# Kernel optimization log

Measured on AMD Instinct MI355X. Metric: run time of the kernel, lower is better.

## Reference

```python
import jax, jax.numpy as jnp
import numpy as np

B, N, K, E = 2, 131072, 20, 256  # batch, points, n_slot, feat/embed dim
GN_GROUPS = 4
IOU_THR = 0.5
SCORE_THR = 0.04
TEMP = 0.05


def setup_inputs() -> dict:
    key = jax.random.key(0)
    ks = jax.random.split(key, 6)
    wscale = 1.0 / np.sqrt(E)
    return {
        "features": jax.random.normal(ks[0], (B, N, E), jnp.float32),
        "slots": jax.random.normal(ks[1], (B, K, E), jnp.float32),
        "w1": jax.random.normal(ks[2], (E, E), jnp.float32) * wscale,
        "b1": jax.random.normal(ks[3], (E,), jnp.float32) * 0.01,
        "gn_g": jnp.ones((E,), jnp.float32),
        "gn_b": jnp.zeros((E,), jnp.float32),
        "w2": jax.random.normal(ks[4], (E, E), jnp.float32) * wscale,
        "b2": jax.random.normal(ks[5], (E,), jnp.float32) * 0.01,
    }


def _l2norm(x, axis):
    n = jnp.linalg.norm(x, axis=axis, keepdims=True)
    return x / jnp.maximum(n, 1e-12)  # F.normalize semantics


def _nms_filter(mask):
    # mask: [N, K] soft instance probabilities (rows sum to 1)
    scores = mask.mean(axis=0)                       # [K]
    valid = scores >= SCORE_THR
    order = jnp.argsort(-scores)                     # descending score
    sm = mask[:, order]                              # [N, K] sorted columns
    bm = (sm > 0.5).astype(mask.dtype).T             # [K, N] binary masks
    areas = bm.sum(axis=1)                           # [K]
    inter = bm @ bm.T                                # [K, K] pairwise intersections
    union = areas[:, None] + areas[None, :] - inter
    iou = inter / (union + 1e-8)
    idx = jnp.arange(K)
    sup0 = ~valid[order]                             # invalid slots pre-suppressed

    def body(i, sup):
        keep_i = ~sup[i]
        return sup | (keep_i & (iou[i] > IOU_THR) & (idx > i))

    sup = jax.lax.fori_loop(0, K, body, sup0)
    kept = ~sup                                      # [K]
    # kept columns are packed (in score order) into the left of the output;
    # dropped columns are routed to a dump column K which is sliced away.
    pos = jnp.cumsum(kept) - 1
    cols = jnp.where(kept, pos, K)
    out = jnp.zeros((mask.shape[0], K + 1), mask.dtype).at[:, cols].set(sm)
    out = out[:, :K]
    # per-point renormalization over kept masks (zeros stay zero if none kept)
    return out / (out.sum(axis=1, keepdims=True) + 1e-8)


def reference(features, slots, w1, b1, gn_g, gn_b, w2, b2):
    # object_mlp: Conv1d(1x1) -> GroupNorm(4) -> ReLU -> Conv1d(1x1)
    x = jnp.einsum('bke,oe->bok', slots, w1) + b1[None, :, None]   # [B, E, K]
    xg = x.reshape(B, GN_GROUPS, E // GN_GROUPS, K)
    mu = xg.mean(axis=(2, 3), keepdims=True)
    var = xg.var(axis=(2, 3), keepdims=True)
    xg = (xg - mu) * jax.lax.rsqrt(var + 1e-5)
    x = xg.reshape(B, E, K) * gn_g[None, :, None] + gn_b[None, :, None]
    x = jax.nn.relu(x)
    slot = jnp.einsum('bek,fe->bfk', x, w2) + b2[None, :, None]    # [B, F=E, K]

    fn = _l2norm(features, axis=-1)                                # [B, N, E]
    sn = _l2norm(slot, axis=1)                                     # [B, E, K]
    logits = jnp.einsum('bnd,bdk->bnk', fn, sn) / TEMP
    mask = jax.nn.softmax(logits, axis=-1)                         # [B, N, K]

    out = jax.vmap(_nms_filter)(mask)                              # [B, N, K]
    return out.transpose(0, 2, 1)                                  # [B, K, N]
```

## Files before the change

### kernel.cpp

```cpp
#include <hip/hip_runtime.h>

#define B_ 2
#define N_ 131072
#define K_ 20
#define E_ 256
#define TEMP_ 0.05f
#define SCORE_THR_ 0.04f

#define WS_SCORE 0
#define WS_XN    1024
#define WS_SN    16384
#define WS_MASK  32768
#define WS_SPART 6291456

typedef __attribute__((ext_vector_type(8))) short short8;
typedef __attribute__((ext_vector_type(4))) float f32x4;

__device__ inline float wave_sum(float v) {
    #pragma unroll
    for (int off = 32; off; off >>= 1) v += __shfl_xor(v, off, 64);
    return v;
}

__device__ inline void cvt_hilo(const float4 a, const float4 b, short8& h, short8& l) {
    float f[8] = {a.x, a.y, a.z, a.w, b.x, b.y, b.z, b.w};
    #pragma unroll
    for (int j = 0; j < 8; ++j) {
        const unsigned u  = __float_as_uint(f[j]);
        const unsigned hb = (u + 0x7fffu + ((u >> 16) & 1u)) & 0xffff0000u;
        h[j] = (short)(hb >> 16);
        const float r = f[j] - __uint_as_float(hb);
        const unsigned v = __float_as_uint(r);
        l[j] = (short)((v + 0x7fffu + ((v >> 16) & 1u)) >> 16);
    }
}

__global__ __launch_bounds__(256) void kA1(const float* __restrict__ slots,
                                           const float* __restrict__ w1,
                                           const float* __restrict__ b1,
                                           const float* __restrict__ gn_g,
                                           const float* __restrict__ gn_b,
                                           float* __restrict__ ws) {
    __shared__ __align__(16) float slds[20 * 260];
    __shared__ float red[2];
    const int t = threadIdx.x;
    const int b = blockIdx.x >> 2, g = blockIdx.x & 3;
    if (t < 2) red[t] = 0.f;
    const float* sb = slots + (size_t)b * K_ * E_;
    #pragma unroll
    for (int i = 0; i < 20; ++i) slds[i * 260 + t] = sb[i * 256 + t];
    __syncthreads();

    const int c = t >> 2, q = t & 3;
    const int o = g * 64 + c;
    const float* w1r = w1 + (size_t)o * E_;
    float acc[5] = {0.f, 0.f, 0.f, 0.f, 0.f};
    for (int e4 = 0; e4 < 64; ++e4) {
        const float4 w4 = *(const float4*)(w1r + e4 * 4);
        #pragma unroll
        for (int kk = 0; kk < 5; ++kk) {
            const float4 s4 = *(const float4*)&slds[(q * 5 + kk) * 260 + e4 * 4];
            acc[kk] += w4.x * s4.x + w4.y * s4.y + w4.z * s4.z + w4.w * s4.w;
        }
    }
    const float bias = b1[o];
    float s1 = 0.f, s2 = 0.f;
    #pragma unroll
    for (int kk = 0; kk < 5; ++kk) {
        acc[kk] += bias;
        s1 += acc[kk];
        s2 += acc[kk] * acc[kk];
    }
    s1 = wave_sum(s1);
    s2 = wave_sum(s2);
    if ((t & 63) == 0) { atomicAdd(&red[0], s1); atomicAdd(&red[1], s2); }
    __syncthreads();
    const float mean = red[0] * (1.f / 1280.f);
    const float var  = red[1] * (1.f / 1280.f) - mean * mean;
    const float rstd = rsqrtf(var + 1e-5f);
    const float gg = gn_g[o], gb = gn_b[o];
    float* xn = ws + WS_XN + (size_t)b * K_ * E_;
    #pragma unroll
    for (int kk = 0; kk < 5; ++kk) {
        float v = (acc[kk] - mean) * rstd * gg + gb;
        v = v > 0.f ? v : 0.f;
        xn[(q * 5 + kk) * 256 + o] = v;
    }
}

__global__ __launch_bounds__(256) void kA2(const float* __restrict__ w2,
                                           const float* __restrict__ b2,
                                           float* __restrict__ ws) {
    __shared__ __align__(16) float xv[256];
    __shared__ float wred[4];
    const int t = threadIdx.x;
    const int b = blockIdx.x / 20, k = blockIdx.x % 20;
    const float* xn = ws + WS_XN + (size_t)(b * 20 + k) * 256;
    xv[t] = xn[t];
    __syncthreads();
    const float* w2r = w2 + (size_t)t * 256;
    float acc = 0.f;
    for (int e4 = 0; e4 < 64; ++e4) {
        const float4 w4 = *(const float4*)(w2r + e4 * 4);
        const float4 x4 = *(const float4*)&xv[e4 * 4];
        acc += w4.x * x4.x + w4.y * x4.y + w4.z * x4.z + w4.w * x4.w;
    }
    acc += b2[t];
    float sq = wave_sum(acc * acc);
    if ((t & 63) == 0) wred[t >> 6] = sq;
    __syncthreads();
    const float nsq = wred[0] + wred[1] + wred[2] + wred[3];
    const float inv = 1.f / fmaxf(sqrtf(nsq), 1e-12f);
    ws[WS_SN + (size_t)(b * 20 + k) * 256 + t] = acc * inv;
}

__global__ __launch_bounds__(256, 2) void kB(const float* __restrict__ feat,
                                             float* __restrict__ ws) {
    __shared__ short8 sfh[2][8][64];
    __shared__ short8 sfl[2][8][64];
    __shared__ float wsum[4][20];
    const int t = threadIdx.x;
    const int lane = t & 63, w = t >> 6;
    const int b = blockIdx.x >> 9, blk = blockIdx.x & 511;
    const int s = lane & 15, g = lane >> 4;

    {
        #pragma unroll
        for (int i = 0; i < 4; ++i) {
            const int combo = w * 4 + i;
            const int tile = combo >> 3, ks = combo & 7;
            const int slot = tile * 16 + s;
            short8 h, l;
            if (slot < K_) {
                const float* snp = ws + WS_SN + ((size_t)(b * K_ + slot)) * E_
                                 + ks * 32 + g * 8;
                cvt_hilo(*(const float4*)snp, *(const float4*)(snp + 4), h, l);
            } else {
                #pragma unroll
                for (int j = 0; j < 8; ++j) { h[j] = 0; l[j] = 0; }
            }
            sfh[tile][ks][lane] = h;
            sfl[tile][ks][lane] = l;
        }
    }
    __syncthreads();

    const float* fp0 = feat + ((size_t)b * N_ + blk * 256 + s) * E_;
    float sreg0 = 0.f, sreg1 = 0.f;

    for (int it = 0; it < 4; ++it) {
        const int pb = w * 64 + it * 16;
        const float* fp = fp0 + (size_t)pb * E_;
        f32x4 c0 = {0.f, 0.f, 0.f, 0.f};
        f32x4 c1 = {0.f, 0.f, 0.f, 0.f};
        float nr = 0.f;
        #pragma unroll
        for (int ks = 0; ks < 8; ++ks) {
            const float* q = fp + ks * 32 + g * 8;
            const float4 a  = *(const float4*)q;
            const float4 bb = *(const float4*)(q + 4);
            nr += a.x * a.x + a.y * a.y + a.z * a.z + a.w * a.w
                + bb.x * bb.x + bb.y * bb.y + bb.z * bb.z + bb.w * bb.w;
            short8 fh, fl;
            cvt_hilo(a, bb, fh, fl);
            const short8 sh0 = sfh[0][ks][lane], sl0 = sfl[0][ks][lane];
            const short8 sh1 = sfh[1][ks][lane], sl1 = sfl[1][ks][lane];
            c0 = __builtin_amdgcn_mfma_f32_16x16x32_bf16(fh, sh0, c0, 0, 0, 0);
            c1 = __builtin_amdgcn_mfma_f32_16x16x32_bf16(fh, sh1, c1, 0, 0, 0);
            c0 = __builtin_amdgcn_mfma_f32_16x16x32_bf16(fh, sl0, c0, 0, 0, 0);
            c1 = __builtin_amdgcn_mfma_f32_16x16x32_bf16(fh, sl1, c1, 0, 0, 0);
            c0 = __builtin_amdgcn_mfma_f32_16x16x32_bf16(fl, sh0, c0, 0, 0, 0);
            c1 = __builtin_amdgcn_mfma_f32_16x16x32_bf16(fl, sh1, c1, 0, 0, 0);
        }
        nr += __shfl_xor(nr, 16, 64);
        nr += __shfl_xor(nr, 32, 64);
        const float scl = rsqrtf(fmaxf(nr, 1e-24f)) * (1.f / TEMP_);

        float p0[4], p1[4];
        #pragma unroll
        for (int r = 0; r < 4; ++r) {
            const float sr = __shfl(scl, 4 * g + r, 64);
            const float x0 = c0[r] * sr;
            const float x1 = c1[r] * sr;
            float m = (s < 4) ? fmaxf(x0, x1) : x0;
            #pragma unroll
            for (int off = 1; off < 16; off <<= 1) m = fmaxf(m, __shfl_xor(m, off, 64));
            const float e0 = __expf(x0 - m);
            const float e1 = (s < 4) ? __expf(x1 - m) : 0.f;
            float su = e0 + e1;
            #pragma unroll
            for (int off = 1; off < 16; off <<= 1) su += __shfl_xor(su, off, 64);
            const float inv = 1.f / su;
            p0[r] = e0 * inv;
            p1[r] = e1 * inv;
        }
        const int col = blk * 256 + pb + 4 * g;
        float* mrow = ws + WS_MASK + ((size_t)b * K_ + s) * N_ + col;
        *(float4*)mrow = make_float4(p0[0], p0[1], p0[2], p0[3]);
        sreg0 += p0[0] + p0[1] + p0[2] + p0[3];
        if (s < 4) {
            float* mrow1 = ws + WS_MASK + ((size_t)b * K_ + 16 + s) * N_ + col;
            *(float4*)mrow1 = make_float4(p1[0], p1[1], p1[2], p1[3]);
            sreg1 += p1[0] + p1[1] + p1[2] + p1[3];
        }
    }

    sreg0 += __shfl_xor(sreg0, 16, 64);
    sreg0 += __shfl_xor(sreg0, 32, 64);
    sreg1 += __shfl_xor(sreg1, 16, 64);
    sreg1 += __shfl_xor(sreg1, 32, 64);
    if (lane < 16) wsum[w][lane] = sreg0;
    if (lane < 4)  wsum[w][16 + lane] = sreg1;
    __syncthreads();
    if (t < 20)
        ws[WS_SPART + (size_t)blockIdx.x * 20 + t] =
            wsum[0][t] + wsum[1][t] + wsum[2][t] + wsum[3][t];
}

__global__ __launch_bounds__(64) void kC(float* __restrict__ ws) {
    const int l = threadIdx.x;
    const int b = blockIdx.x / 20, k = blockIdx.x % 20;
    const float* sp = ws + WS_SPART;
    float sum = 0.f;
    #pragma unroll
    for (int i = 0; i < 8; ++i)
        sum += sp[(size_t)(b * 512 + l + i * 64) * 20 + k];
    sum = wave_sum(sum);
    if (l == 0) ws[WS_SCORE + blockIdx.x] = sum * (1.f / (float)N_);
}

__global__ __launch_bounds__(256) void kD(const float* __restrict__ ws,
                                          float* __restrict__ out) {
    __shared__ float sc[20];
    __shared__ int rnk[20];
    __shared__ int src[20];
    __shared__ int nk_s;
    const int t = threadIdx.x;
    const int b = blockIdx.x >> 9;
    const int n = (blockIdx.x & 511) * 256 + t;
    if (t < 20) sc[t] = ws[WS_SCORE + b * 20 + t];
    if (t == 0) nk_s = 0;
    __syncthreads();
    if (t < 20) {
        const float mys = sc[t];
        int rank = 0;
        for (int j = 0; j < 20; ++j) {
            const float o = sc[j];
            rank += (o > mys) || (o == mys && j < t);
        }
        rnk[t] = rank;
    }
    __syncthreads();
    if (t < 20 && sc[t] >= SCORE_THR_) {
        int pos = 0;
        for (int j = 0; j < 20; ++j)
            pos += (sc[j] >= SCORE_THR_) && (rnk[j] < rnk[t]);
        src[pos] = t;
        atomicAdd(&nk_s, 1);
    }
    __syncthreads();
    const int nk = nk_s;
    const float* mg = ws + WS_MASK + (size_t)b * 20 * N_;
    float mv[20];
    float den = 1e-8f;
    #pragma unroll
    for (int p = 0; p < 20; ++p) {
        float v = 0.f;
        if (p < nk) v = mg[(size_t)src[p] * N_ + n];
        mv[p] = v;
        den += v;
    }
    const float r = 1.f / den;
    float* og = out + (size_t)b * 20 * N_ + n;
    #pragma unroll
    for (int p = 0; p < 20; ++p) og[(size_t)p * N_] = (p < nk) ? mv[p] * r : 0.f;
}

extern "C" void kernel_launch(void* const* d_in, const int* in_sizes, int n_in,
                              void* d_out, int out_size, void* d_ws, size_t ws_size,
                              hipStream_t stream) {
    const float* feat  = (const float*)d_in[0];
    const float* slots = (const float*)d_in[1];
    const float* w1    = (const float*)d_in[2];
    const float* b1    = (const float*)d_in[3];
    const float* gng   = (const float*)d_in[4];
    const float* gnb   = (const float*)d_in[5];
    const float* w2    = (const float*)d_in[6];
    const float* b2    = (const float*)d_in[7];
    float* ws  = (float*)d_ws;
    float* out = (float*)d_out;

    kA1<<<8,    256, 0, stream>>>(slots, w1, b1, gng, gnb, ws);
    kA2<<<40,   256, 0, stream>>>(w2, b2, ws);
    kB <<<1024, 256, 0, stream>>>(feat, ws);
    kC <<<40,   64,  0, stream>>>(ws);
    kD <<<1024, 256, 0, stream>>>(ws, out);
}
```

Before: 423.9 us.

## Stream features through LDS with async global_load_lds double buffering

Per-wave feature loads in kB now go through direct global-to-LDS DMA (global_load_lds) into a double-buffered per-wave LDS tile, issued two quarters ahead, instead of direct float4 global loads. A rotated (swizzled) LDS layout is meant to avoid bank conflicts when reading back the MFMA operand fragments. The aim is to overlap the streaming feature reads, which dominate traffic, with the hi/lo bf16 MFMA work. In exchange it adds 32KB of LDS per block, which may limit occupancy, and relies on hand-placed waitcnt and sched barriers whose correctness depends on the exact count of outstanding loads.

```diff
diff --git a/kernel.cpp b/kernel.cpp
--- a/kernel.cpp
+++ b/kernel.cpp
@@ -20,6 +20,12 @@
     #pragma unroll
     for (int off = 32; off; off >>= 1) v += __shfl_xor(v, off, 64);
     return v;
+}
+
+__device__ inline void dma16(const void* g, void* l) {
+    __builtin_amdgcn_global_load_lds(
+        (const __attribute__((address_space(1))) void*)g,
+        (__attribute__((address_space(3))) void*)l, 16, 0, 0);
 }
 
 __device__ inline void cvt_hilo(const float4 a, const float4 b, short8& h, short8& l) {
@@ -118,6 +124,7 @@
                                              float* __restrict__ ws) {
     __shared__ short8 sfh[2][8][64];
     __shared__ short8 sfl[2][8][64];
+    __shared__ __align__(16) float4 fbuf[4][2][256];
     __shared__ float wsum[4][20];
     const int t = threadIdx.x;
     const int lane = t & 63, w = t >> 6;
@@ -145,32 +152,81 @@
     }
     __syncthreads();
 
-    const float* fp0 = feat + ((size_t)b * N_ + blk * 256 + s) * E_;
+    const int pA = lane >> 3;
+    const int pB = 8 + (lane >> 3);
+    const int loff0 = pA * 1024 + ((((lane & 7) - pA) & 7) << 4);
+    const int loff1 = pB * 1024 + ((((lane & 7) - pB) & 7) << 4);
+    const int loff2 = loff0 + 128;
+    const int loff3 = loff1 + 128;
+    const char* wbase = (const char*)(feat + ((size_t)b * N_ + (size_t)blk * 256 + w * 64) * E_);
+
+    auto issueQ = [&](int qq) {
+        const char* tb = wbase + (qq >> 2) * 16384 + (qq & 3) * 256;
+        float4* db = &fbuf[w][qq & 1][0];
+        dma16(tb + loff0, db);
+        dma16(tb + loff1, db + 64);
+        dma16(tb + loff2, db + 128);
+        dma16(tb + loff3, db + 192);
+    };
+
+    const int ub = ((s >> 3) << 6) + ((s & 7) << 3);
+    const int u00 = ub + ((2 * g + 0 + s) & 7);
+    const int u01 = ub + ((2 * g + 1 + s) & 7);
+    const int u10 = u00 + 128;
+    const int u11 = u01 + 128;
+
+    issueQ(0);
+    issueQ(1);
+
     float sreg0 = 0.f, sreg1 = 0.f;
 
     for (int it = 0; it < 4; ++it) {
         const int pb = w * 64 + it * 16;
-        const float* fp = fp0 + (size_t)pb * E_;
         f32x4 c0 = {0.f, 0.f, 0.f, 0.f};
         f32x4 c1 = {0.f, 0.f, 0.f, 0.f};
         float nr = 0.f;
         #pragma unroll
-        for (int ks = 0; ks < 8; ++ks) {
-            const float* q = fp + ks * 32 + g * 8;
-            const float4 a  = *(const float4*)q;
-            const float4 bb = *(const float4*)(q + 4);
-            nr += a.x * a.x + a.y * a.y + a.z * a.z + a.w * a.w
-                + bb.x * bb.x + bb.y * bb.y + bb.z * bb.z + bb.w * bb.w;
-            short8 fh, fl;
-            cvt_hilo(a, bb, fh, fl);
-            const short8 sh0 = sfh[0][ks][lane], sl0 = sfl[0][ks][lane];
-            const short8 sh1 = sfh[1][ks][lane], sl1 = sfl[1][ks][lane];
-            c0 = __builtin_amdgcn_mfma_f32_16x16x32_bf16(fh, sh0, c0, 0, 0, 0);
-            c1 = __builtin_amdgcn_mfma_f32_16x16x32_bf16(fh, sh1, c1, 0, 0, 0);
-            c0 = __builtin_amdgcn_mfma_f32_16x16x32_bf16(fh, sl0, c0, 0, 0, 0);
-            c1 = __builtin_amdgcn_mfma_f32_16x16x32_bf16(fh, sl1, c1, 0, 0, 0);
-            c0 = __builtin_amdgcn_mfma_f32_16x16x32_bf16(fl, sh0, c0, 0, 0, 0);
-            c1 = __builtin_amdgcn_mfma_f32_16x16x32_bf16(fl, sh1, c1, 0, 0, 0);
+        for (int qi = 0; qi < 4; ++qi) {
+            const int q = it * 4 + qi;
+            if (q < 15) { asm volatile("s_waitcnt vmcnt(4)" ::: "memory"); }
+            else        { asm volatile("s_waitcnt vmcnt(0)" ::: "memory"); }
+            __builtin_amdgcn_sched_barrier(0);
+            const float4* bq = &fbuf[w][q & 1][0];
+            const float4 a0 = bq[u00], b0 = bq[u01];
+            const float4 a1 = bq[u10], b1 = bq[u11];
+            asm volatile("s_waitcnt lgkmcnt(0)" ::: "memory");
+            __builtin_amdgcn_sched_barrier(0);
+            if (q + 2 < 16) issueQ(q + 2);
+            {
+                nr += a0.x*a0.x + a0.y*a0.y + a0.z*a0.z + a0.w*a0.w
+                    + b0.x*b0.x + b0.y*b0.y + b0.z*b0.z + b0.w*b0.w;
+                short8 fh, fl;
+                cvt_hilo(a0, b0, fh, fl);
+                const int ks = qi * 2;
+                const short8 sh0 = sfh[0][ks][lane], sl0 = sfl[0][ks][lane];
+                const short8 sh1 = sfh[1][ks][lane], sl1 = sfl[1][ks][lane];
+                c0 = __builtin_amdgcn_mfma_f32_16x16x32_bf16(fh, sh0, c0, 0, 0, 0);
+                c1 = __builtin_amdgcn_mfma_f32_16x16x32_bf16(fh, sh1, c1, 0, 0, 0);
+                c0 = __builtin_amdgcn_mfma_f32_16x16x32_bf16(fh, sl0, c0, 0, 0, 0);
+                c1 = __builtin_amdgcn_mfma_f32_16x16x32_bf16(fh, sl1, c1, 0, 0, 0);
+                c0 = __builtin_amdgcn_mfma_f32_16x16x32_bf16(fl, sh0, c0, 0, 0, 0);
+                c1 = __builtin_amdgcn_mfma_f32_16x16x32_bf16(fl, sh1, c1, 0, 0, 0);
+            }
+            {
+                nr += a1.x*a1.x + a1.y*a1.y + a1.z*a1.z + a1.w*a1.w
+                    + b1.x*b1.x + b1.y*b1.y + b1.z*b1.z + b1.w*b1.w;
+                short8 fh, fl;
+                cvt_hilo(a1, b1, fh, fl);
+                const int ks = qi * 2 + 1;
+                const short8 sh0 = sfh[0][ks][lane], sl0 = sfl[0][ks][lane];
+                const short8 sh1 = sfh[1][ks][lane], sl1 = sfl[1][ks][lane];
+                c0 = __builtin_amdgcn_mfma_f32_16x16x32_bf16(fh, sh0, c0, 0, 0, 0);
+                c1 = __builtin_amdgcn_mfma_f32_16x16x32_bf16(fh, sh1, c1, 0, 0, 0);
+                c0 = __builtin_amdgcn_mfma_f32_16x16x32_bf16(fh, sl0, c0, 0, 0, 0);
+                c1 = __builtin_amdgcn_mfma_f32_16x16x32_bf16(fh, sl1, c1, 0, 0, 0);
+                c0 = __builtin_amdgcn_mfma_f32_16x16x32_bf16(fl, sh0, c0, 0, 0, 0);
+                c1 = __builtin_amdgcn_mfma_f32_16x16x32_bf16(fl, sh1, c1, 0, 0, 0);
+            }
         }
         nr += __shfl_xor(nr, 16, 64);
         nr += __shfl_xor(nr, 32, 64);
```

Result: no change. 424.5 us (median of 2 runs) (+0.1%).
